# Optimization experiments

Measured on AMD Instinct MI355X. Metric: run time of the kernel, lower is better.

Reference implementation:

```python
import jax, jax.numpy as jnp
import numpy as np

B, T, D, V = 32, 2048, 256, 2048  # batch, time, embed_dim, num_codebooks


def setup_inputs() -> dict:
    key = jax.random.key(0)
    k1, k2 = jax.random.split(key)
    z = jax.random.normal(k1, (B, T, D), dtype=jnp.float32)
    codebook_weight = jax.random.normal(k2, (V, D), dtype=jnp.float32)
    return {"z": z, "codebook_weight": codebook_weight}


def reference(z, codebook_weight):
    # e = codebook.embedding.weight.clone().detach()
    e = jax.lax.stop_gradient(codebook_weight)            # (V, D)
    zf = z.reshape(-1, e.shape[1])                        # (N, D), N = B*T
    # squared euclidean distances via GEMM expansion
    d = (jnp.sum(zf * zf, axis=1, keepdims=True)
         + jnp.sum(e * e, axis=1)
         - 2.0 * zf @ e.T)                                # (N, V)
    idx = jnp.argmin(d, axis=1)                           # (N,)
    # one-hot matmul with e is mathematically a row gather of e
    z_q = jnp.take(e, idx, axis=0).reshape(z.shape)       # (B, T, D)
    commitment_loss = jnp.mean((z - jax.lax.stop_gradient(z_q)) ** 2)
    z_q_st = z + jax.lax.stop_gradient(z_q - z)           # straight-through
    encoding_indices = idx.reshape(z.shape[0], z.shape[1])  # (B, T)
    hist = jnp.bincount(idx, length=V).astype(jnp.float32)
    codebook_prob = hist / (hist.sum() + 1e-8)
    return commitment_loss, z_q_st, encoding_indices, codebook_prob
```

## Files before the change

kernel.cpp:

```cpp
#include <hip/hip_runtime.h>

#define NROWS 65536
#define DIM   256
#define VCB   2048

typedef _Float16 f16;
typedef _Float16 f16x8 __attribute__((ext_vector_type(8)));
typedef float    f32x4 __attribute__((ext_vector_type(4)));


__device__ __forceinline__ void async16(void* lds, const void* g) {
  __builtin_amdgcn_global_load_lds(
      (const __attribute__((address_space(1))) void*)g,
      (__attribute__((address_space(3))) void*)lds, 16, 0, 0);
}

__global__ __launch_bounds__(256) void convert_kernel(
    const float4* __restrict__ src, short4* __restrict__ dhi,
    short4* __restrict__ dlo, int n4) {
  int stride = gridDim.x * 256;
  for (int i = blockIdx.x * 256 + threadIdx.x; i < n4; i += stride) {
    float4 v = src[i];
    union { f16 h[4]; short4 s; } H, L;
    H.h[0] = (f16)v.x; H.h[1] = (f16)v.y; H.h[2] = (f16)v.z; H.h[3] = (f16)v.w;
    L.h[0] = (f16)(v.x - (float)H.h[0]);
    L.h[1] = (f16)(v.y - (float)H.h[1]);
    L.h[2] = (f16)(v.z - (float)H.h[2]);
    L.h[3] = (f16)(v.w - (float)H.h[3]);
    dhi[i] = H.s; dlo[i] = L.s;
  }
}

__global__ __launch_bounds__(256) void prep_kernel(
    const float* __restrict__ e, float* __restrict__ enorm,
    unsigned int* __restrict__ hist, double* __restrict__ loss_part) {
  int tid = threadIdx.x;
  int gt = blockIdx.x * 256 + tid;
  if (gt < VCB) hist[gt] = 0u;
  if (gt < 256) loss_part[gt] = 0.0;
  int wid  = gt >> 6;
  int lane = tid & 63;
  if (wid < VCB) {
    const float4* row = (const float4*)(e + (size_t)wid * DIM);
    float4 v = row[lane];
    float s = v.x*v.x + v.y*v.y + v.z*v.z + v.w*v.w;
    #pragma unroll
    for (int off = 32; off; off >>= 1) s += __shfl_xor(s, off);
    if (lane == 0) enorm[wid] = s;
  }
}

__global__ __launch_bounds__(512) void argmin_kernel(
    const float* __restrict__ z,
    const f16* __restrict__ eh, const f16* __restrict__ el,
    const float* __restrict__ enorm,
    int* __restrict__ idx_out, unsigned int* __restrict__ hist,
    double* __restrict__ loss_part) {
  __shared__ f16 ldsA[8][8192];
  __shared__ f16 ldsB[2][8192];

  const int tid  = threadIdx.x;
  const int wid  = tid >> 6;
  const int lane = tid & 63;
  const int wr   = wid >> 2;
  const int wc   = wid & 3;
  const int lrow = lane & 15;
  const int lq   = lane >> 4;
  const int rbase = blockIdx.x * 128;

  const int srow = tid >> 2;
  const int scol = tid & 3;
  const int skoff = ((scol ^ ((srow >> 1) & 3)) << 3);

  auto stageB = [&](int b, int vcol, int kt) {
    size_t off = (size_t)(vcol + srow) * DIM + (kt << 5) + skoff;
    async16(&ldsB[b][0]    + tid * 8, eh + off);
    async16(&ldsB[b][4096] + tid * 8, el + off);
  };

  {
    const int row = tid >> 2;
    const int q   = tid & 3;
    const float* zrow = z + (size_t)(rbase + row) * DIM + q * 64;
    const int sw = (row >> 1) & 3;
    float zs = 0.f;
    #pragma unroll
    for (int f = 0; f < 16; ++f) {
      float4 v = *(const float4*)(zrow + f * 4);
      int col4   = q * 64 + f * 4;
      int kt     = col4 >> 5;
      int ko     = col4 & 31;
      int chunk  = ko >> 3;
      int within = (ko & 7) * 2;
      int addr = kt * 16384 + row * 64 + ((chunk ^ sw) << 4) + within;
      union { f16 h[4]; short4 s4; } H, L;
      H.h[0] = (f16)v.x; H.h[1] = (f16)v.y; H.h[2] = (f16)v.z; H.h[3] = (f16)v.w;
      L.h[0] = (f16)(v.x - (float)H.h[0]);
      L.h[1] = (f16)(v.y - (float)H.h[1]);
      L.h[2] = (f16)(v.z - (float)H.h[2]);
      L.h[3] = (f16)(v.w - (float)H.h[3]);
      *(short4*)((char*)ldsA + addr)        = H.s4;
      *(short4*)((char*)ldsA + addr + 8192) = L.s4;
      zs += v.x*v.x + v.y*v.y + v.z*v.z + v.w*v.w;
    }
    #pragma unroll
    for (int off = 32; off; off >>= 1) zs += __shfl_xor(zs, off);
    if (lane == 0) atomicAdd(&loss_part[blockIdx.x & 255], (double)zs);
  }
  stageB(0, 0, 0);
  asm volatile("s_waitcnt vmcnt(0)" ::: "memory");
  __syncthreads();

  float minv[4][4];
  int   mini[4][4];
  #pragma unroll
  for (int m = 0; m < 4; ++m)
    #pragma unroll
    for (int r = 0; r < 4; ++r) { minv[m][r] = 3.4e38f; mini[m][r] = 0; }

  const int cchunk = lq ^ ((lrow >> 1) & 3);

  int pb = 0;
  for (int ss = 0; ss < 4; ++ss) {
    const int vt = ss << 9;
    f32x4 acc[4][4][2];
    #pragma unroll
    for (int h = 0; h < 4; ++h)
      #pragma unroll
      for (int m = 0; m < 4; ++m)
        #pragma unroll
        for (int n = 0; n < 2; ++n) {
          f32x4 zz = {0.f, 0.f, 0.f, 0.f};
          acc[h][m][n] = zz;
        }

    f16x8 ah[4], al[4];
    for (int kt = 0; kt < 8; ++kt) {
      #pragma unroll
      for (int h = 0; h < 4; ++h) {
        if (h == 0) {
          const char* abase = (const char*)&ldsA[kt][0];
          #pragma unroll
          for (int m = 0; m < 4; ++m) {
            int row = wr * 64 + m * 16 + lrow;
            int off = row * 64 + cchunk * 16;
            ah[m] = *(const f16x8*)(abase + off);
            al[m] = *(const f16x8*)(abase + 8192 + off);
          }
        }

        bool last = (ss == 3) && (kt == 7) && (h == 3);
        if (!last) {
          int nh = h + 1, nkt = kt, nss = ss;
          if (nh == 4) { nh = 0; ++nkt; if (nkt == 8) { nkt = 0; ++nss; } }
          stageB(pb ^ 1, (nss << 9) + (nh << 7), nkt);
          asm volatile("s_waitcnt vmcnt(2)" ::: "memory");
        } else {
          asm volatile("s_waitcnt vmcnt(0)" ::: "memory");
        }
        asm volatile("s_barrier" ::: "memory");
        __builtin_amdgcn_sched_barrier(0);

        const char* bbase = (const char*)&ldsB[0][0] + pb * 16384;
        #pragma unroll
        for (int n = 0; n < 2; ++n) {
          int col = wc * 32 + n * 16 + lrow;
          int off = col * 64 + cchunk * 16;
          f16x8 bh = *(const f16x8*)(bbase + off);
          f16x8 bl = *(const f16x8*)(bbase + 8192 + off);
          #pragma unroll
          for (int m = 0; m < 4; ++m) {
            acc[h][m][n] = __builtin_amdgcn_mfma_f32_16x16x32_f16(ah[m], bh, acc[h][m][n], 0, 0, 0);
            acc[h][m][n] = __builtin_amdgcn_mfma_f32_16x16x32_f16(ah[m], bl, acc[h][m][n], 0, 0, 0);
            acc[h][m][n] = __builtin_amdgcn_mfma_f32_16x16x32_f16(al[m], bh, acc[h][m][n], 0, 0, 0);
          }
        }
        __builtin_amdgcn_sched_barrier(0);
        asm volatile("s_barrier" ::: "memory");
        pb ^= 1;
      }
    }

    #pragma unroll
    for (int h = 0; h < 4; ++h)
      #pragma unroll
      for (int n = 0; n < 2; ++n) {
        int j = vt + (h << 7) + wc * 32 + n * 16 + lrow;
        float en = enorm[j];
        #pragma unroll
        for (int m = 0; m < 4; ++m)
          #pragma unroll
          for (int r = 0; r < 4; ++r) {
            float s = fmaf(-2.f, acc[h][m][n][r], en);
            if (s < minv[m][r]) { minv[m][r] = s; mini[m][r] = j; }
          }
      }
  }

  #pragma unroll
  for (int off = 1; off < 16; off <<= 1) {
    #pragma unroll
    for (int m = 0; m < 4; ++m)
      #pragma unroll
      for (int r = 0; r < 4; ++r) {
        float ov = __shfl_xor(minv[m][r], off);
        int   oi = __shfl_xor(mini[m][r], off);
        if (ov < minv[m][r] || (ov == minv[m][r] && oi < mini[m][r])) {
          minv[m][r] = ov; mini[m][r] = oi;
        }
      }
  }

  __syncthreads();
  float* sxv = (float*)&ldsB[0][0];
  int*   sxi = (int*)(sxv + 3 * 2 * 64);
  if (wc != 0 && lrow == 0) {
    #pragma unroll
    for (int m = 0; m < 4; ++m)
      #pragma unroll
      for (int r = 0; r < 4; ++r) {
        int li = m * 16 + lq * 4 + r;
        int ix = ((wc - 1) * 2 + wr) * 64 + li;
        sxv[ix] = minv[m][r];
        sxi[ix] = mini[m][r];
      }
  }
  __syncthreads();
  if (wc == 0 && lrow == 0) {
    float lsum = 0.f;
    #pragma unroll
    for (int m = 0; m < 4; ++m)
      #pragma unroll
      for (int r = 0; r < 4; ++r) {
        int li = m * 16 + lq * 4 + r;
        float v  = minv[m][r];
        int   bi = mini[m][r];
        #pragma unroll
        for (int g = 0; g < 3; ++g) {
          int ix = (g * 2 + wr) * 64 + li;
          float ov = sxv[ix];
          int   oi = sxi[ix];
          if (ov < v || (ov == v && oi < bi)) { v = ov; bi = oi; }
        }
        idx_out[rbase + wr * 64 + li] = bi;
        atomicAdd(&hist[bi], 1u);
        lsum += v;
      }
    lsum += __shfl_xor(lsum, 16);
    lsum += __shfl_xor(lsum, 32);
    if (lane == 0) atomicAdd(&loss_part[blockIdx.x & 255], (double)lsum);
  }
}

__global__ __launch_bounds__(256) void gather_kernel(
    const float* __restrict__ e, const int* __restrict__ idx,
    float* __restrict__ zq_out, float* __restrict__ idxf_out) {
  int tid  = threadIdx.x;
  int w    = tid >> 6;
  int lane = tid & 63;
  int n    = blockIdx.x * 4 + w;

  int ci = idx[n];
  const float4* er = (const float4*)(e + (size_t)ci * DIM);
  ((float4*)(zq_out + (size_t)n * DIM))[lane] = er[lane];
  if (lane == 0) idxf_out[n] = (float)ci;
}

__global__ __launch_bounds__(256) void finalize_kernel(
    const unsigned int* __restrict__ hist, const double* __restrict__ loss_part,
    float* __restrict__ out) {
  __shared__ double lsh[4];
  __shared__ float  hsh[4];
  __shared__ float  denom_sh;
  int tid = threadIdx.x, lane = tid & 63, w = tid >> 6;

  float hs = 0.f;
  for (int j = tid; j < VCB; j += 256) hs += (float)hist[j];
  double ls = loss_part[tid];
  #pragma unroll
  for (int off = 32; off; off >>= 1) {
    hs += __shfl_xor(hs, off);
    ls += __shfl_xor(ls, off);
  }
  if (lane == 0) { lsh[w] = ls; hsh[w] = hs; }
  __syncthreads();
  if (tid == 0) {
    double lt = lsh[0] + lsh[1] + lsh[2] + lsh[3];
    float  ht = hsh[0] + hsh[1] + hsh[2] + hsh[3];
    out[0] = (float)(lt / (double)((size_t)NROWS * DIM));
    denom_sh = ht + 1e-8f;
  }
  __syncthreads();
  float denom = denom_sh;
  float* prob = out + 1 + (size_t)NROWS * DIM + NROWS;
  for (int j = tid; j < VCB; j += 256) prob[j] = (float)hist[j] / denom;
}

extern "C" void kernel_launch(void* const* d_in, const int* in_sizes, int n_in,
                              void* d_out, int out_size, void* d_ws, size_t ws_size,
                              hipStream_t stream) {
  (void)in_sizes; (void)n_in; (void)out_size; (void)ws_size;
  const float* z = (const float*)d_in[0];
  const float* e = (const float*)d_in[1];
  float* out = (float*)d_out;
  char*  ws  = (char*)d_ws;

  int*          idx       = (int*)ws;
  unsigned int* hist      = (unsigned int*)(ws + 262144);
  double*       loss_part = (double*)(ws + 270336);
  float*        enorm     = (float*)(ws + 272384);
  f16*          e_hi      = (f16*)(ws + 524288);
  f16*          e_lo      = (f16*)(ws + 1572864);

  float* out_zq  = out + 1;
  float* out_idx = out + 1 + (size_t)NROWS * DIM;

  convert_kernel<<<128, 256, 0, stream>>>(
      (const float4*)e, (short4*)e_hi, (short4*)e_lo, VCB * DIM / 4);
  prep_kernel<<<512, 256, 0, stream>>>(e, enorm, hist, loss_part);
  argmin_kernel<<<NROWS / 128, 512, 0, stream>>>(
      z, e_hi, e_lo, enorm, idx, hist, loss_part);
  gather_kernel<<<NROWS / 4, 256, 0, stream>>>(e, idx, out_zq, out_idx);
  finalize_kernel<<<1, 256, 0, stream>>>(hist, loss_part, out);
}
```

Before: 254.6 us.

## Two-pass argmin: fp16 screening with split-precision recheck of ambiguous rows

The argmin is split into a screening pass that uses only fp16 hi parts, with one MFMA per tile instead of three. It tracks the top-two distances per row and flags any row whose margin is at most a fixed delta. Flagged rows are recomputed in split-precision (hi/lo) by a second kernel over 16 codebook chunks, and a small merge kernel combines the chunk results. Scratch buffers are carved from the output region before the gather overwrites it. This cuts MFMA work for most rows, but correctness depends on the DELTA bound covering the fp16 error, and it adds extra launches and a work list.

```diff
diff --git a/kernel.cpp b/kernel.cpp
--- a/kernel.cpp
+++ b/kernel.cpp
@@ -3,6 +3,7 @@
 #define NROWS 65536
 #define DIM   256
 #define VCB   2048
+#define DELTA 0.25f
 
 typedef _Float16 f16;
 typedef _Float16 f16x8 __attribute__((ext_vector_type(8)));
@@ -33,9 +34,11 @@
 
 __global__ __launch_bounds__(256) void prep_kernel(
     const float* __restrict__ e, float* __restrict__ enorm,
-    unsigned int* __restrict__ hist, double* __restrict__ loss_part) {
+    unsigned int* __restrict__ hist, double* __restrict__ loss_part,
+    int* __restrict__ flag_cnt) {
   int tid = threadIdx.x;
   int gt = blockIdx.x * 256 + tid;
+  if (gt == 0) flag_cnt[0] = 0;
   if (gt < VCB) hist[gt] = 0u;
   if (gt < 256) loss_part[gt] = 0.0;
   int wid  = gt >> 6;
@@ -50,14 +53,17 @@
   }
 }
 
-__global__ __launch_bounds__(512) void argmin_kernel(
-    const float* __restrict__ z,
-    const f16* __restrict__ eh, const f16* __restrict__ el,
+__global__ __launch_bounds__(512) void pass1_kernel(
+    const float* __restrict__ z, const f16* __restrict__ eh,
     const float* __restrict__ enorm,
     int* __restrict__ idx_out, unsigned int* __restrict__ hist,
-    double* __restrict__ loss_part) {
-  __shared__ f16 ldsA[8][8192];
-  __shared__ f16 ldsB[2][8192];
+    double* __restrict__ loss_part,
+    int* __restrict__ flag_cnt, int* __restrict__ flag_list) {
+  __shared__ f16 ldsA[8][4096];
+  __shared__ f16 ldsB[2][16384];
+  __shared__ float sx1[3][2][64];
+  __shared__ float sx2[3][2][64];
+  __shared__ int   sxi[3][2][64];
 
   const int tid  = threadIdx.x;
   const int wid  = tid >> 6;
@@ -72,10 +78,12 @@
   const int scol = tid & 3;
   const int skoff = ((scol ^ ((srow >> 1) & 3)) << 3);
 
-  auto stageB = [&](int b, int vcol, int kt) {
-    size_t off = (size_t)(vcol + srow) * DIM + (kt << 5) + skoff;
-    async16(&ldsB[b][0]    + tid * 8, eh + off);
-    async16(&ldsB[b][4096] + tid * 8, el + off);
+  auto stageB = [&](int b, int ss, int kh) {
+    #pragma unroll
+    for (int s = 0; s < 4; ++s) {
+      size_t goff = (size_t)(ss * 128 + srow) * DIM + kh * 128 + s * 32 + skoff;
+      async16(&ldsB[b][s * 4096] + tid * 8, eh + goff);
+    }
   };
 
   {
@@ -92,15 +100,10 @@
       int ko     = col4 & 31;
       int chunk  = ko >> 3;
       int within = (ko & 7) * 2;
-      int addr = kt * 16384 + row * 64 + ((chunk ^ sw) << 4) + within;
-      union { f16 h[4]; short4 s4; } H, L;
+      int addr = kt * 8192 + row * 64 + ((chunk ^ sw) << 4) + within;
+      union { f16 h[4]; short4 s4; } H;
       H.h[0] = (f16)v.x; H.h[1] = (f16)v.y; H.h[2] = (f16)v.z; H.h[3] = (f16)v.w;
-      L.h[0] = (f16)(v.x - (float)H.h[0]);
-      L.h[1] = (f16)(v.y - (float)H.h[1]);
-      L.h[2] = (f16)(v.z - (float)H.h[2]);
-      L.h[3] = (f16)(v.w - (float)H.h[3]);
-      *(short4*)((char*)ldsA + addr)        = H.s4;
-      *(short4*)((char*)ldsA + addr + 8192) = L.s4;
+      *(short4*)((char*)ldsA + addr) = H.s4;
       zs += v.x*v.x + v.y*v.y + v.z*v.z + v.w*v.w;
     }
     #pragma unroll
@@ -111,90 +114,76 @@
   asm volatile("s_waitcnt vmcnt(0)" ::: "memory");
   __syncthreads();
 
-  float minv[4][4];
-  int   mini[4][4];
+  float m1[4][4], m2v[4][4];
+  int   i1[4][4];
   #pragma unroll
   for (int m = 0; m < 4; ++m)
     #pragma unroll
-    for (int r = 0; r < 4; ++r) { minv[m][r] = 3.4e38f; mini[m][r] = 0; }
+    for (int r = 0; r < 4; ++r) { m1[m][r] = 3.4e38f; m2v[m][r] = 3.4e38f; i1[m][r] = 0; }
 
   const int cchunk = lq ^ ((lrow >> 1) & 3);
 
   int pb = 0;
-  for (int ss = 0; ss < 4; ++ss) {
-    const int vt = ss << 9;
-    f32x4 acc[4][4][2];
-    #pragma unroll
-    for (int h = 0; h < 4; ++h)
-      #pragma unroll
-      for (int m = 0; m < 4; ++m)
-        #pragma unroll
-        for (int n = 0; n < 2; ++n) {
-          f32x4 zz = {0.f, 0.f, 0.f, 0.f};
-          acc[h][m][n] = zz;
-        }
-
-    f16x8 ah[4], al[4];
-    for (int kt = 0; kt < 8; ++kt) {
-      #pragma unroll
-      for (int h = 0; h < 4; ++h) {
-        if (h == 0) {
-          const char* abase = (const char*)&ldsA[kt][0];
-          #pragma unroll
-          for (int m = 0; m < 4; ++m) {
-            int row = wr * 64 + m * 16 + lrow;
-            int off = row * 64 + cchunk * 16;
-            ah[m] = *(const f16x8*)(abase + off);
-            al[m] = *(const f16x8*)(abase + 8192 + off);
-          }
-        }
-
-        bool last = (ss == 3) && (kt == 7) && (h == 3);
-        if (!last) {
-          int nh = h + 1, nkt = kt, nss = ss;
-          if (nh == 4) { nh = 0; ++nkt; if (nkt == 8) { nkt = 0; ++nss; } }
-          stageB(pb ^ 1, (nss << 9) + (nh << 7), nkt);
-          asm volatile("s_waitcnt vmcnt(2)" ::: "memory");
-        } else {
-          asm volatile("s_waitcnt vmcnt(0)" ::: "memory");
-        }
-        asm volatile("s_barrier" ::: "memory");
-        __builtin_amdgcn_sched_barrier(0);
-
-        const char* bbase = (const char*)&ldsB[0][0] + pb * 16384;
+  for (int ss = 0; ss < 16; ++ss) {
+    f32x4 acc[4][2];
+    #pragma unroll
+    for (int m = 0; m < 4; ++m)
+      #pragma unroll
+      for (int n = 0; n < 2; ++n) {
+        f32x4 zz = {0.f, 0.f, 0.f, 0.f};
+        acc[m][n] = zz;
+      }
+
+    for (int kh = 0; kh < 2; ++kh) {
+      bool last = (ss == 15) && (kh == 1);
+      if (!last) {
+        int nkh = kh + 1, nss = ss;
+        if (nkh == 2) { nkh = 0; ++nss; }
+        stageB(pb ^ 1, nss, nkh);
+        asm volatile("s_waitcnt vmcnt(4)" ::: "memory");
+      } else {
+        asm volatile("s_waitcnt vmcnt(0)" ::: "memory");
+      }
+      asm volatile("s_barrier" ::: "memory");
+      __builtin_amdgcn_sched_barrier(0);
+
+      #pragma unroll
+      for (int kp = 0; kp < 4; ++kp) {
+        const char* abase = (const char*)&ldsA[kh * 4 + kp][0];
+        f16x8 ah[4];
+        #pragma unroll
+        for (int m = 0; m < 4; ++m) {
+          int row = wr * 64 + m * 16 + lrow;
+          ah[m] = *(const f16x8*)(abase + row * 64 + cchunk * 16);
+        }
+        const char* bbase = (const char*)&ldsB[pb][kp * 4096];
         #pragma unroll
         for (int n = 0; n < 2; ++n) {
           int col = wc * 32 + n * 16 + lrow;
-          int off = col * 64 + cchunk * 16;
-          f16x8 bh = *(const f16x8*)(bbase + off);
-          f16x8 bl = *(const f16x8*)(bbase + 8192 + off);
+          f16x8 bh = *(const f16x8*)(bbase + col * 64 + cchunk * 16);
           #pragma unroll
-          for (int m = 0; m < 4; ++m) {
-            acc[h][m][n] = __builtin_amdgcn_mfma_f32_16x16x32_f16(ah[m], bh, acc[h][m][n], 0, 0, 0);
-            acc[h][m][n] = __builtin_amdgcn_mfma_f32_16x16x32_f16(ah[m], bl, acc[h][m][n], 0, 0, 0);
-            acc[h][m][n] = __builtin_amdgcn_mfma_f32_16x16x32_f16(al[m], bh, acc[h][m][n], 0, 0, 0);
-          }
-        }
-        __builtin_amdgcn_sched_barrier(0);
-        asm volatile("s_barrier" ::: "memory");
-        pb ^= 1;
-      }
-    }
-
-    #pragma unroll
-    for (int h = 0; h < 4; ++h)
-      #pragma unroll
-      for (int n = 0; n < 2; ++n) {
-        int j = vt + (h << 7) + wc * 32 + n * 16 + lrow;
-        float en = enorm[j];
-        #pragma unroll
-        for (int m = 0; m < 4; ++m)
-          #pragma unroll
-          for (int r = 0; r < 4; ++r) {
-            float s = fmaf(-2.f, acc[h][m][n][r], en);
-            if (s < minv[m][r]) { minv[m][r] = s; mini[m][r] = j; }
-          }
-      }
+          for (int m = 0; m < 4; ++m)
+            acc[m][n] = __builtin_amdgcn_mfma_f32_16x16x32_f16(ah[m], bh, acc[m][n], 0, 0, 0);
+        }
+      }
+      __builtin_amdgcn_sched_barrier(0);
+      asm volatile("s_barrier" ::: "memory");
+      pb ^= 1;
+    }
+
+    #pragma unroll
+    for (int n = 0; n < 2; ++n) {
+      int j = ss * 128 + wc * 32 + n * 16 + lrow;
+      float en = enorm[j];
+      #pragma unroll
+      for (int m = 0; m < 4; ++m)
+        #pragma unroll
+        for (int r = 0; r < 4; ++r) {
+          float s = fmaf(-2.f, acc[m][n][r], en);
+          if (s < m1[m][r]) { m2v[m][r] = m1[m][r]; m1[m][r] = s; i1[m][r] = j; }
+          else if (s < m2v[m][r]) m2v[m][r] = s;
+        }
+    }
   }
 
   #pragma unroll
@@ -203,26 +192,26 @@
     for (int m = 0; m < 4; ++m)
       #pragma unroll
       for (int r = 0; r < 4; ++r) {
-        float ov = __shfl_xor(minv[m][r], off);
-        int   oi = __shfl_xor(mini[m][r], off);
-        if (ov < minv[m][r] || (ov == minv[m][r] && oi < mini[m][r])) {
-          minv[m][r] = ov; mini[m][r] = oi;
-        }
-      }
-  }
-
-  __syncthreads();
-  float* sxv = (float*)&ldsB[0][0];
-  int*   sxi = (int*)(sxv + 3 * 2 * 64);
+        float o1 = __shfl_xor(m1[m][r], off);
+        int   oi = __shfl_xor(i1[m][r], off);
+        float o2 = __shfl_xor(m2v[m][r], off);
+        float nm2 = fminf(fminf(m2v[m][r], o2), fmaxf(m1[m][r], o1));
+        if (o1 < m1[m][r] || (o1 == m1[m][r] && oi < i1[m][r])) {
+          m1[m][r] = o1; i1[m][r] = oi;
+        }
+        m2v[m][r] = nm2;
+      }
+  }
+
   if (wc != 0 && lrow == 0) {
     #pragma unroll
     for (int m = 0; m < 4; ++m)
       #pragma unroll
       for (int r = 0; r < 4; ++r) {
         int li = m * 16 + lq * 4 + r;
-        int ix = ((wc - 1) * 2 + wr) * 64 + li;
-        sxv[ix] = minv[m][r];
-        sxi[ix] = mini[m][r];
+        sx1[wc - 1][wr][li] = m1[m][r];
+        sx2[wc - 1][wr][li] = m2v[m][r];
+        sxi[wc - 1][wr][li] = i1[m][r];
       }
   }
   __syncthreads();
@@ -233,22 +222,242 @@
       #pragma unroll
       for (int r = 0; r < 4; ++r) {
         int li = m * 16 + lq * 4 + r;
-        float v  = minv[m][r];
-        int   bi = mini[m][r];
+        float v  = m1[m][r];
+        int   bi = i1[m][r];
+        float v2 = m2v[m][r];
         #pragma unroll
         for (int g = 0; g < 3; ++g) {
-          int ix = (g * 2 + wr) * 64 + li;
-          float ov = sxv[ix];
-          int   oi = sxi[ix];
+          float ov = sx1[g][wr][li];
+          float o2 = sx2[g][wr][li];
+          int   oi = sxi[g][wr][li];
+          float nm2 = fminf(fminf(v2, o2), fmaxf(v, ov));
           if (ov < v || (ov == v && oi < bi)) { v = ov; bi = oi; }
-        }
-        idx_out[rbase + wr * 64 + li] = bi;
-        atomicAdd(&hist[bi], 1u);
-        lsum += v;
+          v2 = nm2;
+        }
+        int row = rbase + wr * 64 + li;
+        if (v2 - v <= DELTA) {
+          int p = atomicAdd(flag_cnt, 1);
+          flag_list[p] = row;
+        } else {
+          idx_out[row] = bi;
+          atomicAdd(&hist[bi], 1u);
+          lsum += v;
+        }
       }
     lsum += __shfl_xor(lsum, 16);
     lsum += __shfl_xor(lsum, 32);
     if (lane == 0) atomicAdd(&loss_part[blockIdx.x & 255], (double)lsum);
+  }
+}
+
+__global__ __launch_bounds__(512) void pass2_kernel(
+    const float* __restrict__ z,
+    const f16* __restrict__ eh, const f16* __restrict__ el,
+    const float* __restrict__ enorm,
+    const int* __restrict__ flag_cnt, const int* __restrict__ flag_list,
+    float* __restrict__ pval, int* __restrict__ pidx) {
+  __shared__ f16 ldsA[8][8192];
+  __shared__ f16 ldsB[2][8192];
+
+  const int tid  = threadIdx.x;
+  const int wid  = tid >> 6;
+  const int lane = tid & 63;
+  const int wr   = wid >> 2;
+  const int wc   = wid & 3;
+  const int lrow = lane & 15;
+  const int lq   = lane >> 4;
+  const int srow = tid >> 2;
+  const int scol = tid & 3;
+  const int skoff = ((scol ^ ((srow >> 1) & 3)) << 3);
+  const int cchunk = lq ^ ((lrow >> 1) & 3);
+  const int cnt = *flag_cnt;
+
+  auto stageB = [&](int b, int vcol, int kt) {
+    size_t off = (size_t)(vcol + srow) * DIM + (kt << 5) + skoff;
+    async16(&ldsB[b][0]    + tid * 8, eh + off);
+    async16(&ldsB[b][4096] + tid * 8, el + off);
+  };
+
+  for (int job = blockIdx.x; ; job += gridDim.x) {
+    int chunk = job >> 4, cb = job & 15;
+    int base = chunk * 128;
+    if (base >= cnt) break;
+    int nrows = cnt - base; if (nrows > 128) nrows = 128;
+
+    __syncthreads();
+
+    {
+      const int row = tid >> 2;
+      const int q   = tid & 3;
+      int grow = flag_list[base + (row < nrows ? row : 0)];
+      const float* zrow = z + (size_t)grow * DIM + q * 64;
+      const int sw = (row >> 1) & 3;
+      #pragma unroll
+      for (int f = 0; f < 16; ++f) {
+        float4 v = *(const float4*)(zrow + f * 4);
+        int col4   = q * 64 + f * 4;
+        int kt     = col4 >> 5;
+        int ko     = col4 & 31;
+        int chunk2 = ko >> 3;
+        int within = (ko & 7) * 2;
+        int addr = kt * 16384 + row * 64 + ((chunk2 ^ sw) << 4) + within;
+        union { f16 h[4]; short4 s4; } H, L;
+        H.h[0] = (f16)v.x; H.h[1] = (f16)v.y; H.h[2] = (f16)v.z; H.h[3] = (f16)v.w;
+        L.h[0] = (f16)(v.x - (float)H.h[0]);
+        L.h[1] = (f16)(v.y - (float)H.h[1]);
+        L.h[2] = (f16)(v.z - (float)H.h[2]);
+        L.h[3] = (f16)(v.w - (float)H.h[3]);
+        *(short4*)((char*)ldsA + addr)        = H.s4;
+        *(short4*)((char*)ldsA + addr + 8192) = L.s4;
+      }
+    }
+    int pb = 0;
+    stageB(0, cb * 128, 0);
+    asm volatile("s_waitcnt vmcnt(0)" ::: "memory");
+    __syncthreads();
+
+    float minv[4][4];
+    int   mini[4][4];
+    #pragma unroll
+    for (int m = 0; m < 4; ++m)
+      #pragma unroll
+      for (int r = 0; r < 4; ++r) { minv[m][r] = 3.4e38f; mini[m][r] = 0; }
+
+    f32x4 acc[4][2];
+    #pragma unroll
+    for (int m = 0; m < 4; ++m)
+      #pragma unroll
+      for (int n = 0; n < 2; ++n) {
+        f32x4 zz = {0.f, 0.f, 0.f, 0.f};
+        acc[m][n] = zz;
+      }
+
+    for (int kt = 0; kt < 8; ++kt) {
+      if (kt < 7) {
+        stageB(pb ^ 1, cb * 128, kt + 1);
+        asm volatile("s_waitcnt vmcnt(2)" ::: "memory");
+      } else {
+        asm volatile("s_waitcnt vmcnt(0)" ::: "memory");
+      }
+      asm volatile("s_barrier" ::: "memory");
+      __builtin_amdgcn_sched_barrier(0);
+
+      const char* abase = (const char*)&ldsA[kt][0];
+      f16x8 ah[4], al[4];
+      #pragma unroll
+      for (int m = 0; m < 4; ++m) {
+        int row = wr * 64 + m * 16 + lrow;
+        int off = row * 64 + cchunk * 16;
+        ah[m] = *(const f16x8*)(abase + off);
+        al[m] = *(const f16x8*)(abase + 8192 + off);
+      }
+      const char* bbase = (const char*)&ldsB[pb][0];
+      #pragma unroll
+      for (int n = 0; n < 2; ++n) {
+        int col = wc * 32 + n * 16 + lrow;
+        int off = col * 64 + cchunk * 16;
+        f16x8 bh = *(const f16x8*)(bbase + off);
+        f16x8 bl = *(const f16x8*)(bbase + 8192 + off);
+        #pragma unroll
+        for (int m = 0; m < 4; ++m) {
+          acc[m][n] = __builtin_amdgcn_mfma_f32_16x16x32_f16(ah[m], bh, acc[m][n], 0, 0, 0);
+          acc[m][n] = __builtin_amdgcn_mfma_f32_16x16x32_f16(ah[m], bl, acc[m][n], 0, 0, 0);
+          acc[m][n] = __builtin_amdgcn_mfma_f32_16x16x32_f16(al[m], bh, acc[m][n], 0, 0, 0);
+        }
+      }
+      __builtin_amdgcn_sched_barrier(0);
+      asm volatile("s_barrier" ::: "memory");
+      pb ^= 1;
+    }
+
+    #pragma unroll
+    for (int n = 0; n < 2; ++n) {
+      int j = cb * 128 + wc * 32 + n * 16 + lrow;
+      float en = enorm[j];
+      #pragma unroll
+      for (int m = 0; m < 4; ++m)
+        #pragma unroll
+        for (int r = 0; r < 4; ++r) {
+          float s = fmaf(-2.f, acc[m][n][r], en);
+          if (s < minv[m][r]) { minv[m][r] = s; mini[m][r] = j; }
+        }
+    }
+
+    #pragma unroll
+    for (int off = 1; off < 16; off <<= 1) {
+      #pragma unroll
+      for (int m = 0; m < 4; ++m)
+        #pragma unroll
+        for (int r = 0; r < 4; ++r) {
+          float ov = __shfl_xor(minv[m][r], off);
+          int   oi = __shfl_xor(mini[m][r], off);
+          if (ov < minv[m][r] || (ov == minv[m][r] && oi < mini[m][r])) {
+            minv[m][r] = ov; mini[m][r] = oi;
+          }
+        }
+    }
+
+    __syncthreads();
+    float* sxv = (float*)&ldsB[0][0];
+    int*   sxi2 = (int*)(sxv + 3 * 2 * 64);
+    if (wc != 0 && lrow == 0) {
+      #pragma unroll
+      for (int m = 0; m < 4; ++m)
+        #pragma unroll
+        for (int r = 0; r < 4; ++r) {
+          int li = m * 16 + lq * 4 + r;
+          int ix = ((wc - 1) * 2 + wr) * 64 + li;
+          sxv[ix] = minv[m][r];
+          sxi2[ix] = mini[m][r];
+        }
+    }
+    __syncthreads();
+    if (wc == 0 && lrow == 0) {
+      #pragma unroll
+      for (int m = 0; m < 4; ++m)
+        #pragma unroll
+        for (int r = 0; r < 4; ++r) {
+          int li = m * 16 + lq * 4 + r;
+          float v  = minv[m][r];
+          int   bi = mini[m][r];
+          #pragma unroll
+          for (int g = 0; g < 3; ++g) {
+            int ix = (g * 2 + wr) * 64 + li;
+            float ov = sxv[ix];
+            int   oi = sxi2[ix];
+            if (ov < v || (ov == v && oi < bi)) { v = ov; bi = oi; }
+          }
+          int i = wr * 64 + li;
+          if (i < nrows) {
+            int fi = base + i;
+            pval[fi * 16 + cb] = v;
+            pidx[fi * 16 + cb] = bi;
+          }
+        }
+    }
+  }
+}
+
+__global__ __launch_bounds__(256) void pass2m_kernel(
+    const int* __restrict__ flag_cnt, const int* __restrict__ flag_list,
+    const float* __restrict__ pval, const int* __restrict__ pidx,
+    int* __restrict__ idx_out, unsigned int* __restrict__ hist,
+    double* __restrict__ loss_part) {
+  int cnt = *flag_cnt;
+  int t = blockIdx.x * 256 + threadIdx.x;
+  int stride = gridDim.x * 256;
+  for (int fi = t; fi < cnt; fi += stride) {
+    float m = 3.4e38f; int bi = 0;
+    #pragma unroll
+    for (int cb = 0; cb < 16; ++cb) {
+      float v = pval[fi * 16 + cb];
+      int  ix = pidx[fi * 16 + cb];
+      if (v < m || (v == m && ix < bi)) { m = v; bi = ix; }
+    }
+    int row = flag_list[fi];
+    idx_out[row] = bi;
+    atomicAdd(&hist[bi], 1u);
+    atomicAdd(&loss_part[fi & 255], (double)m);
   }
 }
 
@@ -309,17 +518,26 @@
   unsigned int* hist      = (unsigned int*)(ws + 262144);
   double*       loss_part = (double*)(ws + 270336);
   float*        enorm     = (float*)(ws + 272384);
+  int*          flag_cnt  = (int*)(ws + 280576);
   f16*          e_hi      = (f16*)(ws + 524288);
   f16*          e_lo      = (f16*)(ws + 1572864);
 
+  float* pval      = out + 32;
+  int*   pidx      = (int*)(out + 32 + 1048576);
+  int*   flag_list = (int*)(out + 32 + 2097152);
+
   float* out_zq  = out + 1;
   float* out_idx = out + 1 + (size_t)NROWS * DIM;
 
   convert_kernel<<<128, 256, 0, stream>>>(
       (const float4*)e, (short4*)e_hi, (short4*)e_lo, VCB * DIM / 4);
-  prep_kernel<<<512, 256, 0, stream>>>(e, enorm, hist, loss_part);
-  argmin_kernel<<<NROWS / 128, 512, 0, stream>>>(
-      z, e_hi, e_lo, enorm, idx, hist, loss_part);
+  prep_kernel<<<512, 256, 0, stream>>>(e, enorm, hist, loss_part, flag_cnt);
+  pass1_kernel<<<NROWS / 128, 512, 0, stream>>>(
+      z, e_hi, enorm, idx, hist, loss_part, flag_cnt, flag_list);
+  pass2_kernel<<<512, 512, 0, stream>>>(
+      z, e_hi, e_lo, enorm, flag_cnt, flag_list, pval, pidx);
+  pass2m_kernel<<<64, 256, 0, stream>>>(
+      flag_cnt, flag_list, pval, pidx, idx, hist, loss_part);
   gather_kernel<<<NROWS / 4, 256, 0, stream>>>(e, idx, out_zq, out_idx);
   finalize_kernel<<<1, 256, 0, stream>>>(hist, loss_part, out);
 }
```

After: 222.4 us. -12.7%, faster.
